# Kernel optimization log

Measured on AMD Instinct MI355X. Metric: run time of the kernel, lower is better.

Reference implementation:

```python
import jax, jax.numpy as jnp
import numpy as np

K = 20
EPS = 1e-5
SLOPE = 0.2


def knn_idx(x, k):
    # x: (B, C, N) -> (B, N, k) indices of k nearest neighbors (incl. self)
    xx = jnp.sum(x * x, axis=1)  # (B, N)
    # negative squared distance: largest = nearest
    pd = 2.0 * jnp.einsum('bcn,bcm->bnm', x, x) - xx[:, :, None] - xx[:, None, :]
    return jax.lax.top_k(pd, k)[1]


def graph_feature(x, k):
    # x: (B, C, N) -> (B, 2C, N, k) edge features [x_j - x_i, x_i]
    idx = knn_idx(x, k)                       # (B, N, k)
    xt = jnp.transpose(x, (0, 2, 1))          # (B, N, C)
    feat = jax.vmap(lambda xb, ib: xb[ib])(xt, idx)  # (B, N, k, C)
    center = xt[:, :, None, :]
    out = jnp.concatenate([feat - center, jnp.broadcast_to(center, feat.shape)], axis=-1)
    return jnp.transpose(out, (0, 3, 1, 2))   # (B, 2C, N, k)


def conv_bn_lrelu2d(x, W, g, b):
    # 1x1 Conv2d (no bias) + BatchNorm2d (batch stats, train mode) + LeakyReLU(0.2)
    y = jnp.einsum('oc,bcnk->bonk', W, x)
    m = jnp.mean(y, axis=(0, 2, 3), keepdims=True)
    v = jnp.var(y, axis=(0, 2, 3), keepdims=True)
    y = (y - m) * jax.lax.rsqrt(v + EPS) * g[None, :, None, None] + b[None, :, None, None]
    return jnp.where(y > 0, y, SLOPE * y)


def conv_bn_lrelu1d(x, W, g, b):
    y = jnp.einsum('oc,bcn->bon', W, x)
    m = jnp.mean(y, axis=(0, 2), keepdims=True)
    v = jnp.var(y, axis=(0, 2), keepdims=True)
    y = (y - m) * jax.lax.rsqrt(v + EPS) * g[None, :, None] + b[None, :, None]
    return jnp.where(y > 0, y, SLOPE * y)


def setup_inputs() -> dict:
    key = jax.random.key(0)
    ks = jax.random.split(key, 8)
    B, N, C = 8, 2048, 3
    emb = 1024
    fix = 1  # output == 'pointwise'
    xyz = jax.random.normal(ks[0], (B, N, C), dtype=jnp.float32)
    def w(k, o, i):
        return jax.random.normal(k, (o, i), dtype=jnp.float32) * (1.0 / np.sqrt(i))
    inp = {
        'xyz': xyz,
        'W1': w(ks[1], 64, 2 * C), 'g1': jnp.ones((64,), jnp.float32), 'b1': jnp.zeros((64,), jnp.float32),
        'W2': w(ks[2], 64, 128), 'g2': jnp.ones((64,), jnp.float32), 'b2': jnp.zeros((64,), jnp.float32),
        'W3': w(ks[3], 128, 128), 'g3': jnp.ones((128,), jnp.float32), 'b3': jnp.zeros((128,), jnp.float32),
        'W4': w(ks[4], 256 + fix, 256), 'g4': jnp.ones((256 + fix,), jnp.float32), 'b4': jnp.zeros((256 + fix,), jnp.float32),
        'W5': w(ks[5], emb, 512 + fix), 'g5': jnp.ones((emb,), jnp.float32), 'b5': jnp.zeros((emb,), jnp.float32),
    }
    return inp


def reference(xyz, W1, g1, b1, W2, g2, b2, W3, g3, b3, W4, g4, b4, W5, g5, b5):
    x0 = jnp.transpose(xyz, (0, 2, 1))  # (B, 3, N)
    B, _, N = x0.shape

    x = graph_feature(x0, K)            # (B, 6, N, k)
    x1 = jnp.max(conv_bn_lrelu2d(x, W1, g1, b1), axis=-1)   # (B, 64, N)

    x = graph_feature(x1, K)            # (B, 128, N, k)
    x2 = jnp.max(conv_bn_lrelu2d(x, W2, g2, b2), axis=-1)   # (B, 64, N)

    x = graph_feature(x2, K)            # (B, 128, N, k)
    x3 = jnp.max(conv_bn_lrelu2d(x, W3, g3, b3), axis=-1)   # (B, 128, N)

    x = graph_feature(x3, K)            # (B, 256, N, k)
    x4 = jnp.max(conv_bn_lrelu2d(x, W4, g4, b4), axis=-1)   # (B, 257, N)

    x_f = jnp.concatenate([x1, x2, x3, x4], axis=1)          # (B, 513, N)
    _x = conv_bn_lrelu1d(x_f, W5, g5, b5)                    # (B, emb, N)

    gmax = jnp.max(_x, axis=-1)   # (B, emb)
    gavg = jnp.mean(_x, axis=-1)  # (B, emb)
    g = jnp.concatenate([gmax, gavg], axis=1)[:, :, None]    # (B, 2*emb, 1)
    g = jnp.broadcast_to(g, (B, g.shape[1], N))
    return jnp.concatenate([g, x0, x_f], axis=1)             # (B, 2*emb+3+513, N)
```

## Files before the change

kernel.cpp:

```cpp
#include <hip/hip_runtime.h>
#include <math.h>

#define BB 8
#define NN 2048
#define KK 20
#define OCH 2564
#define OCN ((size_t)OCH*NN)
#define EPSD 1e-5
#define SLOPED 0.2
#define TS 64

#define WS_PD   ((size_t)0)
#define WS_YMX  ((size_t)4194304)
#define WS_YMN  ((size_t)8404992)
#define WS_U    ((size_t)12615680)
#define WS_V    ((size_t)16826368)
#define WS_IDX  ((size_t)21037056)
#define WS_XX   ((size_t)21364736)
#define WS_WTF  ((size_t)21381120)
#define WS_WTD  ((size_t)21426496)
#define WS_W5T  ((size_t)21471872)
#define WS_Y5   ((size_t)0)
#define WS_S1   ((size_t)21997184)
#define WS_S2   (WS_S1 + 2048)
#define WS_SC   (WS_S2 + 2048)
#define WS_SH   (WS_SC + 2048)

static inline int cdiv(int a, int b){ return (a+b-1)/b; }

__global__ void k_prep_x0(const float* __restrict__ xyz, float* __restrict__ out){
  int id = blockIdx.x*256 + threadIdx.x;
  if (id >= BB*NN) return;
  int b = id / NN, n = id % NN;
  const float* p = xyz + ((size_t)b*NN + n)*3;
  float* o = out + (size_t)b*OCN + (size_t)2048*NN + n;
  o[0] = p[0]; o[(size_t)NN] = p[1]; o[2*(size_t)NN] = p[2];
}

__global__ void k_wt_all(const float* __restrict__ W1, const float* __restrict__ W2,
                         const float* __restrict__ W3, const float* __restrict__ W4,
                         const float* __restrict__ W5,
                         float* __restrict__ wtf, float* __restrict__ wtd,
                         float* __restrict__ w5t){
  int id = blockIdx.x*256 + threadIdx.x;
  if (id < 513*1024){
    int c = id / 1024, o = id % 1024;
    w5t[(size_t)c*1024 + o] = W5[(size_t)o*513 + c];
  }
  if (id < 45376){
    const float* W; int C, O; int base;
    if (id < 192)        { W = W1; C = 3;   O = 64;  base = 0; }
    else if (id < 4288)  { W = W2; C = 64;  O = 64;  base = 192; }
    else if (id < 12480) { W = W3; C = 64;  O = 128; base = 4288; }
    else                 { W = W4; C = 128; O = 257; base = 12480; }
    int r = id - base;
    int c = r / O, o = r % O;
    float wf = W[(size_t)o*(2*C) + c];
    float wc = W[(size_t)o*(2*C) + C + c];
    wtf[base + (size_t)c*O + o] = wf;
    wtd[base + (size_t)c*O + o] = wc - wf;
  }
}

__global__ void k_xx32(const float* __restrict__ x, int C, size_t bs, float* __restrict__ xx,
                       double* __restrict__ s1, double* __restrict__ s2){
  if (blockIdx.x == 0 && blockIdx.y == 0){
    int t = threadIdx.x;
    #pragma unroll
    for (int i=0;i<4;i++){ s1[t*4+i] = 0.0; s2[t*4+i] = 0.0; }
  }
  int b = blockIdx.y;
  int n = blockIdx.x*256 + threadIdx.x;
  const float* p = x + (size_t)b*bs + n;
  float a;
  if (C <= 8){
    a = 0.f;
    for (int c = 0; c < C; c++){ float v = p[(size_t)c*NN]; float s = v*v; a = a + s; }
  } else {
    float r0,r1,r2,r3,r4,r5,r6,r7;
    { float v;
      v = p[0];            r0 = v*v;
      v = p[(size_t)1*NN]; r1 = v*v;
      v = p[(size_t)2*NN]; r2 = v*v;
      v = p[(size_t)3*NN]; r3 = v*v;
      v = p[(size_t)4*NN]; r4 = v*v;
      v = p[(size_t)5*NN]; r5 = v*v;
      v = p[(size_t)6*NN]; r6 = v*v;
      v = p[(size_t)7*NN]; r7 = v*v;
    }
    for (int i = 8; i < C; i += 8){
      float v;
      v = p[(size_t)(i+0)*NN]; r0 = r0 + v*v;
      v = p[(size_t)(i+1)*NN]; r1 = r1 + v*v;
      v = p[(size_t)(i+2)*NN]; r2 = r2 + v*v;
      v = p[(size_t)(i+3)*NN]; r3 = r3 + v*v;
      v = p[(size_t)(i+4)*NN]; r4 = r4 + v*v;
      v = p[(size_t)(i+5)*NN]; r5 = r5 + v*v;
      v = p[(size_t)(i+6)*NN]; r6 = r6 + v*v;
      v = p[(size_t)(i+7)*NN]; r7 = r7 + v*v;
    }
    a = ((r0+r1)+(r2+r3)) + ((r4+r5)+(r6+r7));
  }
  xx[b*NN + n] = a;
}

__global__ __launch_bounds__(256) void k_pd4(const float* __restrict__ x, int C, size_t bs, int b0,
                     const float* __restrict__ xx, float* __restrict__ wsbase,
                     unsigned long long o0, unsigned long long o1,
                     unsigned long long o2, unsigned long long o3){
  int z = blockIdx.z;
  unsigned long long off = (z==0)?o0:((z==1)?o1:((z==2)?o2:o3));
  float* pd = wsbase + off;
  int b = b0 + z;
  __shared__ float As[8][128];
  __shared__ float Bs[8][128];
  int n0 = blockIdx.y*128, m0 = blockIdx.x*128;
  int tid = threadIdx.x;
  int ty = tid / 16, tx = tid % 16;
  const float* xb = x + (size_t)b*bs;
  float acc[8][8] = {};
  for (int c0 = 0; c0 < C; c0 += 8){
    #pragma unroll
    for (int rr = 0; rr < 4; rr++){
      int t2 = tid + rr*256;
      int c = t2 >> 7, col = t2 & 127;
      int cc = c0 + c;
      float av = 0.f, bv = 0.f;
      if (cc < C){ av = xb[(size_t)cc*NN + n0 + col]; bv = xb[(size_t)cc*NN + m0 + col]; }
      As[c][col] = av; Bs[c][col] = bv;
    }
    __syncthreads();
    #pragma unroll
    for (int c = 0; c < 8; c++){
      float4 a0 = *reinterpret_cast<const float4*>(&As[c][ty*8]);
      float4 a1 = *reinterpret_cast<const float4*>(&As[c][ty*8+4]);
      float4 b0v = *reinterpret_cast<const float4*>(&Bs[c][tx*4]);
      float4 b1v = *reinterpret_cast<const float4*>(&Bs[c][64 + tx*4]);
      float a[8]  = {a0.x,a0.y,a0.z,a0.w,a1.x,a1.y,a1.z,a1.w};
      float bv[8] = {b0v.x,b0v.y,b0v.z,b0v.w,b1v.x,b1v.y,b1v.z,b1v.w};
      #pragma unroll
      for (int i=0;i<8;i++)
        #pragma unroll
        for (int j=0;j<8;j++)
          acc[i][j] = fmaf(a[i], bv[j], acc[i][j]);
    }
    __syncthreads();
  }
  const float* xxb = xx + b*NN;
  float xm0[4], xm1[4];
  #pragma unroll
  for (int j=0;j<4;j++){ xm0[j] = xxb[m0 + tx*4 + j]; xm1[j] = xxb[m0 + 64 + tx*4 + j]; }
  #pragma unroll
  for (int i=0;i<8;i++){
    int n = n0 + ty*8 + i;
    float xn = xxb[n];
    float4 v0, v1;
    v0.x = (2.f*acc[i][0] - xn) - xm0[0];
    v0.y = (2.f*acc[i][1] - xn) - xm0[1];
    v0.z = (2.f*acc[i][2] - xn) - xm0[2];
    v0.w = (2.f*acc[i][3] - xn) - xm0[3];
    v1.x = (2.f*acc[i][4] - xn) - xm1[0];
    v1.y = (2.f*acc[i][5] - xn) - xm1[1];
    v1.z = (2.f*acc[i][6] - xn) - xm1[2];
    v1.w = (2.f*acc[i][7] - xn) - xm1[3];
    *reinterpret_cast<float4*>(&pd[(size_t)n*NN + m0 + tx*4])      = v0;
    *reinterpret_cast<float4*>(&pd[(size_t)n*NN + m0 + 64 + tx*4]) = v1;
  }
}

__global__ __launch_bounds__(256) void k_topk4(const float* __restrict__ wsbase,
                     unsigned long long o0, unsigned long long o1,
                     unsigned long long o2, unsigned long long o3,
                     int b0, int* __restrict__ idx){
  int z = blockIdx.y;
  unsigned long long off = (z==0)?o0:((z==1)?o1:((z==2)?o2:o3));
  const float* pdb = wsbase + off;
  int b = b0 + z;
  int lane = threadIdx.x & 63;
  int w = threadIdx.x >> 6;
  int n = blockIdx.x*4 + w;
  const float* row = pdb + (size_t)n*NN;
  float vals[KK]; int inds[KK];
  #pragma unroll
  for (int i=0;i<KK;i++){ vals[i] = -INFINITY; inds[i] = NN; }
  for (int c = 0; c < NN/64; c++){
    int m = c*64 + lane;
    float v = row[m];
    if (v > vals[KK-1]){
      #pragma unroll
      for (int i=KK-1;i>0;--i){
        if (vals[i-1] < v){ vals[i]=vals[i-1]; inds[i]=inds[i-1]; }
      }
      bool done = false;
      #pragma unroll
      for (int i=0;i<KK;i++){
        bool pl = (!done) && (vals[i] < v);
        if (pl){ vals[i]=v; inds[i]=m; done=true; }
      }
    }
  }
  int* op = idx + ((size_t)b*NN + n)*KK;
  #pragma unroll 1
  for (int r = 0; r < KK; r++){
    float bv = vals[0]; int bi = inds[0];
    #pragma unroll
    for (int s = 1; s < 64; s <<= 1){
      float ov = __shfl_xor(bv, s);
      int   oi = __shfl_xor(bi, s);
      if (ov > bv || (ov == bv && oi < bi)){ bv = ov; bi = oi; }
    }
    if (inds[0] == bi){
      #pragma unroll
      for (int i=0;i<KK-1;i++){ vals[i]=vals[i+1]; inds[i]=inds[i+1]; }
      vals[KK-1] = -INFINITY; inds[KK-1] = NN;
    }
    if (lane == 0) op[r] = bi;
  }
}

__global__ __launch_bounds__(256) void k_gemm_uv(
    const float* __restrict__ x, int C, int O, size_t bs,
    const float* __restrict__ wtf, const float* __restrict__ wtd,
    float* __restrict__ u, float* __restrict__ v){
  __shared__ float Xs[8][TS];
  __shared__ float Wfs[8][TS];
  __shared__ float Wds[8][TS];
  int b = blockIdx.z;
  int n0 = blockIdx.y*TS, o0 = blockIdx.x*TS;
  int tid = threadIdx.x, tx = tid%16, ty = tid/16;
  const float* xb = x + (size_t)b*bs;
  double au[4][4] = {};
  double av[4][4] = {};
  for (int c0 = 0; c0 < C; c0 += 8){
    int r = tid/64, col = tid%64;
    #pragma unroll
    for (int rr=0;rr<2;rr++){
      int c = c0 + r + rr*4;
      float xv=0.f, wfv=0.f, wdv=0.f;
      if (c < C){
        xv = xb[(size_t)c*NN + n0 + col];
        if (o0+col < O){
          wfv = wtf[(size_t)c*O + o0+col];
          wdv = wtd[(size_t)c*O + o0+col];
        }
      }
      Xs[r+rr*4][col]=xv; Wfs[r+rr*4][col]=wfv; Wds[r+rr*4][col]=wdv;
    }
    __syncthreads();
    #pragma unroll
    for (int c=0;c<8;c++){
      double a[4], f[4], d[4];
      #pragma unroll
      for (int i=0;i<4;i++) a[i] = (double)Xs[c][ty*4+i];
      #pragma unroll
      for (int j=0;j<4;j++) f[j] = (double)Wfs[c][tx*4+j];
      #pragma unroll
      for (int j=0;j<4;j++) d[j] = (double)Wds[c][tx*4+j];
      #pragma unroll
      for (int i=0;i<4;i++)
        #pragma unroll
        for (int j=0;j<4;j++){
          au[i][j] = fma(a[i], f[j], au[i][j]);
          av[i][j] = fma(a[i], d[j], av[i][j]);
        }
    }
    __syncthreads();
  }
  #pragma unroll
  for (int i=0;i<4;i++){
    int n = n0 + ty*4 + i;
    #pragma unroll
    for (int j=0;j<4;j++){
      int o = o0 + tx*4 + j;
      if (o < O){
        u[((size_t)b*NN + n)*O + o] = (float)au[i][j];
        v[((size_t)b*NN + n)*O + o] = (float)av[i][j];
      }
    }
  }
}

#define NT 32
__global__ __launch_bounds__(256) void k_passB(
  const float* __restrict__ u, const float* __restrict__ v, const int* __restrict__ idx,
  int O, int OT, float* __restrict__ ymax, float* __restrict__ ymin,
  double* __restrict__ s1, double* __restrict__ s2){
  __shared__ int ids[NT*KK];
  int b = blockIdx.y, n0 = blockIdx.x*NT;
  int tid = threadIdx.x;
  for (int t = tid; t < NT*KK; t += 256) ids[t] = idx[((size_t)b*NN + n0)*KK + t];
  __syncthreads();
  int nsplit = 256/OT;
  int ob = tid % OT, ns = tid / OT;
  int nper = NT / nsplit;
  const float* ub = u + (size_t)b*NN*O;
  const float* vb = v + (size_t)b*NN*O;
  for (int o = ob; o < O; o += 256){
    double s1p = 0.0, s2p = 0.0;
    for (int ni = ns*nper; ni < (ns+1)*nper; ni++){
      double su=0.0, sq=0.0;
      float mx=-INFINITY, mn=INFINITY;
      #pragma unroll
      for (int k=0;k<KK;k++){
        int j = ids[ni*KK + k];
        float uu = ub[(size_t)j*O + o];
        double ud = (double)uu;
        su += ud; sq += ud*ud;
        mx = fmaxf(mx, uu); mn = fminf(mn, uu);
      }
      float vv = vb[(size_t)(n0+ni)*O + o];
      double vd = (double)vv;
      s1p += su + (double)KK*vd;
      s2p += sq + 2.0*vd*su + (double)KK*vd*vd;
      size_t yo = ((size_t)b*NN + n0 + ni)*O + o;
      ymax[yo] = mx + vv; ymin[yo] = mn + vv;
    }
    atomicAdd(&s1[o], s1p);
    atomicAdd(&s2[o], s2p);
  }
}

__global__ __launch_bounds__(256) void k_passD(const float* __restrict__ ymax,
  const float* __restrict__ ymin, const double* __restrict__ s1,
  const double* __restrict__ s2, const float* __restrict__ g,
  const float* __restrict__ bb, int O, double M, float* __restrict__ xout){
  __shared__ float t[64][65];
  __shared__ double s_sc[64], s_sh[64];
  int b = blockIdx.z, n0 = blockIdx.y*64, o0 = blockIdx.x*64;
  int tid = threadIdx.x;
  if (tid < 64){
    int o = o0 + tid;
    double sc = 0.0, sh = 0.0;
    if (o < O){
      double mean = s1[o]/M;
      double var  = s2[o]/M - mean*mean;
      sc = (double)g[o] / sqrt(var + EPSD);
      sh = (double)bb[o] - mean*sc;
    }
    s_sc[tid] = sc; s_sh[tid] = sh;
  }
  __syncthreads();
  int col = tid % 64, rr = tid / 64;
  int o = o0 + col;
  bool ov = (o < O);
  double sc = s_sc[col];
  double sh = s_sh[col];
  const float* src = (sc >= 0.0) ? ymax : ymin;
  for (int p = 0; p < 16; p++){
    int n = n0 + p*4 + rr;
    float y = ov ? src[((size_t)b*NN + n)*O + o] : 0.f;
    double z = sc*(double)y + sh;
    z = z > 0.0 ? z : SLOPED*z;
    t[p*4+rr][col] = (float)z;
  }
  __syncthreads();
  float* xb = xout + (size_t)b*OCN;
  for (int p = 0; p < 16; p++){
    int row = p*4 + rr;
    if (o0 + row < O) xb[(size_t)(o0+row)*NN + n0 + col] = t[col][row];
  }
}

__global__ __launch_bounds__(256) void k_conv5g(const float* __restrict__ xf,
                                                const float* __restrict__ w5t,
                                                float* __restrict__ y5){
  __shared__ float Wsh[8][128];
  __shared__ float Xs[8][128];
  int o0 = blockIdx.x*128, n0 = blockIdx.y*128, b = blockIdx.z;
  int tid = threadIdx.x;
  int ty = tid / 16, tx = tid % 16;
  const float* xb = xf + (size_t)b*OCN;
  float acc[8][8] = {};
  for (int c0 = 0; c0 < 513; c0 += 8){
    #pragma unroll
    for (int rr = 0; rr < 4; rr++){
      int t2 = tid + rr*256;
      int c = t2 >> 7, col = t2 & 127;
      int cc = c0 + c;
      float wv = 0.f, xv = 0.f;
      if (cc < 513){
        wv = w5t[(size_t)cc*1024 + o0 + col];
        xv = xb[(size_t)cc*NN + n0 + col];
      }
      Wsh[c][col] = wv; Xs[c][col] = xv;
    }
    __syncthreads();
    #pragma unroll
    for (int c = 0; c < 8; c++){
      float4 w0 = *reinterpret_cast<const float4*>(&Wsh[c][ty*8]);
      float4 w1 = *reinterpret_cast<const float4*>(&Wsh[c][ty*8+4]);
      float4 x0 = *reinterpret_cast<const float4*>(&Xs[c][tx*4]);
      float4 x1 = *reinterpret_cast<const float4*>(&Xs[c][64 + tx*4]);
      float wr[8] = {w0.x,w0.y,w0.z,w0.w,w1.x,w1.y,w1.z,w1.w};
      float xr[8] = {x0.x,x0.y,x0.z,x0.w,x1.x,x1.y,x1.z,x1.w};
      #pragma unroll
      for (int i=0;i<8;i++)
        #pragma unroll
        for (int j=0;j<8;j++)
          acc[i][j] = fmaf(wr[i], xr[j], acc[i][j]);
    }
    __syncthreads();
  }
  #pragma unroll
  for (int i=0;i<8;i++){
    int o = o0 + ty*8 + i;
    float* yr = y5 + ((size_t)b*1024 + o)*NN;
    float4 v0 = {acc[i][0], acc[i][1], acc[i][2], acc[i][3]};
    float4 v1 = {acc[i][4], acc[i][5], acc[i][6], acc[i][7]};
    *reinterpret_cast<float4*>(&yr[n0 + tx*4])      = v0;
    *reinterpret_cast<float4*>(&yr[n0 + 64 + tx*4]) = v1;
  }
}

__global__ __launch_bounds__(256) void k_stats5_v2(const float* __restrict__ y5,
                                                   const float* __restrict__ g,
                                                   const float* __restrict__ bb,
                                                   double* __restrict__ scale,
                                                   double* __restrict__ shift){
  int o = blockIdx.x;
  __shared__ double sh1[256], sh2[256];
  double a = 0.0, q = 0.0;
  for (int bn = threadIdx.x; bn < BB*NN; bn += 256){
    int b = bn >> 11, n = bn & 2047;
    double yv = (double)y5[((size_t)b*1024 + o)*NN + n];
    a += yv; q += yv*yv;
  }
  sh1[threadIdx.x] = a; sh2[threadIdx.x] = q;
  __syncthreads();
  for (int s = 128; s > 0; s >>= 1){
    if (threadIdx.x < s){ sh1[threadIdx.x] += sh1[threadIdx.x+s]; sh2[threadIdx.x] += sh2[threadIdx.x+s]; }
    __syncthreads();
  }
  if (threadIdx.x == 0){
    double M = (double)(BB*NN);
    double mean = sh1[0]/M;
    double var  = sh2[0]/M - mean*mean;
    double sc = (double)g[o]/sqrt(var + EPSD);
    scale[o] = sc;
    shift[o] = (double)bb[o] - mean*sc;
  }
}

__global__ __launch_bounds__(256) void k_final5_v2(const float* __restrict__ y5,
                                                   const double* __restrict__ scale,
                                                   const double* __restrict__ shift,
                                                   float* __restrict__ out){
  int o = blockIdx.x, b = blockIdx.y;
  __shared__ double smx[256], ssm[256];
  double sc = scale[o], sh = shift[o];
  double mx = -INFINITY, sm = 0.0;
  const float* yrow = y5 + ((size_t)b*1024 + o)*NN;
  for (int n = threadIdx.x; n < NN; n += 256){
    double z = sc*(double)yrow[n] + sh;
    z = z > 0.0 ? z : SLOPED*z;
    mx = fmax(mx, z); sm += z;
  }
  smx[threadIdx.x] = mx; ssm[threadIdx.x] = sm;
  __syncthreads();
  for (int s = 128; s > 0; s >>= 1){
    if (threadIdx.x < s){
      smx[threadIdx.x] = fmax(smx[threadIdx.x], smx[threadIdx.x+s]);
      ssm[threadIdx.x] += ssm[threadIdx.x+s];
    }
    __syncthreads();
  }
  float vg = (float)smx[0];
  float va = (float)(ssm[0]*(1.0/NN));
  float* ob = out + (size_t)b*OCN;
  for (int n = threadIdx.x; n < NN; n += 256){
    ob[(size_t)o*NN + n] = vg;
    ob[(size_t)(1024+o)*NN + n] = va;
  }
}

extern "C" void kernel_launch(void* const* d_in, const int* in_sizes, int n_in,
                              void* d_out, int out_size, void* d_ws, size_t ws_size,
                              hipStream_t stream){
  const float* xyz = (const float*)d_in[0];
  float* out = (float*)d_out;
  float* ws  = (float*)d_ws;

  const float* Wp[5] = {(const float*)d_in[1],(const float*)d_in[4],(const float*)d_in[7],(const float*)d_in[10],(const float*)d_in[13]};
  const float* Gp[5] = {(const float*)d_in[2],(const float*)d_in[5],(const float*)d_in[8],(const float*)d_in[11],(const float*)d_in[14]};
  const float* Bp[5] = {(const float*)d_in[3],(const float*)d_in[6],(const float*)d_in[9],(const float*)d_in[12],(const float*)d_in[15]};
  int Cin[4]  = {3, 64, 64, 128};
  int Oc[4]   = {64, 64, 128, 257};
  int xinc[4] = {2048, 2051, 2115, 2179};
  int xoutc[4]= {2051, 2115, 2179, 2307};
  int woff[4] = {0, 192, 4288, 12480};

  float* ymx  = ws + WS_YMX;
  float* ymn  = ws + WS_YMN;
  float* u    = ws + WS_U;
  float* v    = ws + WS_V;
  int*   idx  = (int*)(ws + WS_IDX);
  float* xx   = ws + WS_XX;
  float* wtf  = ws + WS_WTF;
  float* wtd  = ws + WS_WTD;
  float* w5t  = ws + WS_W5T;
  float* y5   = ws + WS_Y5;
  double* s1d = (double*)(ws + WS_S1);
  double* s2d = (double*)(ws + WS_S2);
  double* scd = (double*)(ws + WS_SC);
  double* shd = (double*)(ws + WS_SH);

  k_prep_x0<<<cdiv(BB*NN,256), 256, 0, stream>>>(xyz, out);
  k_wt_all <<<cdiv(513*1024,256), 256, 0, stream>>>(Wp[0], Wp[1], Wp[2], Wp[3], Wp[4], wtf, wtd, w5t);

  for (int t = 0; t < 4; t++){
    int C = Cin[t], O = Oc[t];
    const float* xin = out + (size_t)xinc[t]*NN;
    k_xx32<<<dim3(NN/256, BB), 256, 0, stream>>>(xin, C, OCN, xx, s1d, s2d);
    int OT = (O <= 64) ? 64 : ((O <= 128) ? 128 : 256);
    for (int bg = 0; bg < 2; bg++){
      k_pd4  <<<dim3(NN/128, NN/128, 4), 256, 0, stream>>>(xin, C, OCN, bg*4, xx, ws,
               (unsigned long long)WS_PD, (unsigned long long)WS_YMX,
               (unsigned long long)WS_YMN, (unsigned long long)WS_U);
      k_topk4<<<dim3(NN/4, 4), 256, 0, stream>>>(ws,
               (unsigned long long)WS_PD, (unsigned long long)WS_YMX,
               (unsigned long long)WS_YMN, (unsigned long long)WS_U,
               bg*4, idx);
    }
    k_gemm_uv<<<dim3(cdiv(O,TS), NN/TS, BB), 256, 0, stream>>>(xin, C, O, OCN, wtf + woff[t], wtd + woff[t], u, v);
    k_passB  <<<dim3(NN/NT, BB), 256, 0, stream>>>(u, v, idx, O, OT, ymx, ymn, s1d, s2d);
    k_passD  <<<dim3(cdiv(O,TS), NN/TS, BB), 256, 0, stream>>>(ymx, ymn, s1d, s2d, Gp[t], Bp[t], O,
               (double)((size_t)BB*NN*KK), out + (size_t)xoutc[t]*NN);
  }

  k_conv5g<<<dim3(1024/128, NN/128, BB), 256, 0, stream>>>(out + (size_t)2051*NN, w5t, y5);
  k_stats5_v2<<<1024, 256, 0, stream>>>(y5, Gp[4], Bp[4], scd, shd);
  k_final5_v2<<<dim3(1024, BB), 256, 0, stream>>>(y5, scd, shd, out);
}
```

Baseline: 2.422 ms.

## Fuse pairwise-distance GEMM with top-k selection into one kernel

Replaces the two-kernel path, which wrote full NxN distance matrices for groups of four batches and then scanned them for top-k, with a single kernel. Each block computes distances for 32 rows against all columns and keeps per-thread top-k lists in registers, merging them with an 8-lane shuffle reduction. This removes the large distance-matrix write and re-read and one launch per batch group. In exchange the GEMM tiling is less efficient (a 32-row tile with one A value per thread per step, Bs reloaded for every column chunk), the grid is only 512 blocks, and the insertion sort now sits inside the compute loop, which may cause divergence.

```diff
diff --git a/kernel.cpp b/kernel.cpp
--- a/kernel.cpp
+++ b/kernel.cpp
@@ -10,7 +10,6 @@
 #define SLOPED 0.2
 #define TS 64
 
-#define WS_PD   ((size_t)0)
 #define WS_YMX  ((size_t)4194304)
 #define WS_YMN  ((size_t)8404992)
 #define WS_U    ((size_t)12615680)
@@ -104,107 +103,89 @@
   xx[b*NN + n] = a;
 }
 
-__global__ __launch_bounds__(256) void k_pd4(const float* __restrict__ x, int C, size_t bs, int b0,
-                     const float* __restrict__ xx, float* __restrict__ wsbase,
-                     unsigned long long o0, unsigned long long o1,
-                     unsigned long long o2, unsigned long long o3){
-  int z = blockIdx.z;
-  unsigned long long off = (z==0)?o0:((z==1)?o1:((z==2)?o2:o3));
-  float* pd = wsbase + off;
-  int b = b0 + z;
-  __shared__ float As[8][128];
-  __shared__ float Bs[8][128];
-  int n0 = blockIdx.y*128, m0 = blockIdx.x*128;
+__global__ __launch_bounds__(256) void k_pdtopk(
+    const float* __restrict__ x, int C, size_t bs,
+    const float* __restrict__ xx, int* __restrict__ idx){
+  __shared__ float As[128][32];
+  __shared__ float Bs[8][256];
+  int b = blockIdx.y;
+  int r0 = blockIdx.x * 32;
   int tid = threadIdx.x;
-  int ty = tid / 16, tx = tid % 16;
+  int row = tid >> 3;
+  int mc  = tid & 7;
   const float* xb = x + (size_t)b*bs;
-  float acc[8][8] = {};
-  for (int c0 = 0; c0 < C; c0 += 8){
-    #pragma unroll
-    for (int rr = 0; rr < 4; rr++){
-      int t2 = tid + rr*256;
-      int c = t2 >> 7, col = t2 & 127;
-      int cc = c0 + c;
-      float av = 0.f, bv = 0.f;
-      if (cc < C){ av = xb[(size_t)cc*NN + n0 + col]; bv = xb[(size_t)cc*NN + m0 + col]; }
-      As[c][col] = av; Bs[c][col] = bv;
-    }
-    __syncthreads();
-    #pragma unroll
-    for (int c = 0; c < 8; c++){
-      float4 a0 = *reinterpret_cast<const float4*>(&As[c][ty*8]);
-      float4 a1 = *reinterpret_cast<const float4*>(&As[c][ty*8+4]);
-      float4 b0v = *reinterpret_cast<const float4*>(&Bs[c][tx*4]);
-      float4 b1v = *reinterpret_cast<const float4*>(&Bs[c][64 + tx*4]);
-      float a[8]  = {a0.x,a0.y,a0.z,a0.w,a1.x,a1.y,a1.z,a1.w};
-      float bv[8] = {b0v.x,b0v.y,b0v.z,b0v.w,b1v.x,b1v.y,b1v.z,b1v.w};
-      #pragma unroll
-      for (int i=0;i<8;i++)
-        #pragma unroll
-        for (int j=0;j<8;j++)
-          acc[i][j] = fmaf(a[i], bv[j], acc[i][j]);
-    }
-    __syncthreads();
-  }
   const float* xxb = xx + b*NN;
-  float xm0[4], xm1[4];
-  #pragma unroll
-  for (int j=0;j<4;j++){ xm0[j] = xxb[m0 + tx*4 + j]; xm1[j] = xxb[m0 + 64 + tx*4 + j]; }
-  #pragma unroll
-  for (int i=0;i<8;i++){
-    int n = n0 + ty*8 + i;
-    float xn = xxb[n];
-    float4 v0, v1;
-    v0.x = (2.f*acc[i][0] - xn) - xm0[0];
-    v0.y = (2.f*acc[i][1] - xn) - xm0[1];
-    v0.z = (2.f*acc[i][2] - xn) - xm0[2];
-    v0.w = (2.f*acc[i][3] - xn) - xm0[3];
-    v1.x = (2.f*acc[i][4] - xn) - xm1[0];
-    v1.y = (2.f*acc[i][5] - xn) - xm1[1];
-    v1.z = (2.f*acc[i][6] - xn) - xm1[2];
-    v1.w = (2.f*acc[i][7] - xn) - xm1[3];
-    *reinterpret_cast<float4*>(&pd[(size_t)n*NN + m0 + tx*4])      = v0;
-    *reinterpret_cast<float4*>(&pd[(size_t)n*NN + m0 + 64 + tx*4]) = v1;
-  }
-}
-
-__global__ __launch_bounds__(256) void k_topk4(const float* __restrict__ wsbase,
-                     unsigned long long o0, unsigned long long o1,
-                     unsigned long long o2, unsigned long long o3,
-                     int b0, int* __restrict__ idx){
-  int z = blockIdx.y;
-  unsigned long long off = (z==0)?o0:((z==1)?o1:((z==2)?o2:o3));
-  const float* pdb = wsbase + off;
-  int b = b0 + z;
-  int lane = threadIdx.x & 63;
-  int w = threadIdx.x >> 6;
-  int n = blockIdx.x*4 + w;
-  const float* row = pdb + (size_t)n*NN;
+  int Cpad = (C + 7) & ~7;
+  for (int t2 = tid; t2 < Cpad*32; t2 += 256){
+    int c = t2 >> 5, r = t2 & 31;
+    As[c][r] = (c < C) ? xb[(size_t)c*NN + r0 + r] : 0.f;
+  }
+  __syncthreads();
+  float xn = xxb[r0 + row];
   float vals[KK]; int inds[KK];
   #pragma unroll
   for (int i=0;i<KK;i++){ vals[i] = -INFINITY; inds[i] = NN; }
-  for (int c = 0; c < NN/64; c++){
-    int m = c*64 + lane;
-    float v = row[m];
-    if (v > vals[KK-1]){
-      #pragma unroll
-      for (int i=KK-1;i>0;--i){
-        if (vals[i-1] < v){ vals[i]=vals[i-1]; inds[i]=inds[i-1]; }
-      }
-      bool done = false;
-      #pragma unroll
-      for (int i=0;i<KK;i++){
-        bool pl = (!done) && (vals[i] < v);
-        if (pl){ vals[i]=v; inds[i]=m; done=true; }
-      }
-    }
-  }
-  int* op = idx + ((size_t)b*NN + n)*KK;
+  for (int mb = 0; mb < 8; mb++){
+    int mbase = mb*256;
+    float acc[8][4];
+    #pragma unroll
+    for (int q=0;q<8;q++){
+      #pragma unroll
+      for (int e=0;e<4;e++) acc[q][e] = 0.f;
+    }
+    for (int c0 = 0; c0 < C; c0 += 8){
+      #pragma unroll
+      for (int rr=0; rr<8; rr++){
+        int t2 = tid + rr*256;
+        int c = t2 >> 8, col = t2 & 255;
+        int cc = c0 + c;
+        Bs[c][col] = (cc < C) ? xb[(size_t)cc*NN + mbase + col] : 0.f;
+      }
+      __syncthreads();
+      #pragma unroll
+      for (int c=0;c<8;c++){
+        float a = As[c0+c][row];
+        #pragma unroll
+        for (int q=0;q<8;q++){
+          float4 bq = *reinterpret_cast<const float4*>(&Bs[c][q*32 + mc*4]);
+          acc[q][0] = fmaf(a, bq.x, acc[q][0]);
+          acc[q][1] = fmaf(a, bq.y, acc[q][1]);
+          acc[q][2] = fmaf(a, bq.z, acc[q][2]);
+          acc[q][3] = fmaf(a, bq.w, acc[q][3]);
+        }
+      }
+      __syncthreads();
+    }
+    #pragma unroll
+    for (int q=0;q<8;q++){
+      float4 xm = *reinterpret_cast<const float4*>(&xxb[mbase + q*32 + mc*4]);
+      float xmv[4] = {xm.x, xm.y, xm.z, xm.w};
+      #pragma unroll
+      for (int e=0;e<4;e++){
+        float t = 2.f*acc[q][e];
+        float v = (t - xn) - xmv[e];
+        if (v > vals[KK-1]){
+          int m = mbase + q*32 + mc*4 + e;
+          #pragma unroll
+          for (int i=KK-1;i>0;--i){
+            if (vals[i-1] < v){ vals[i]=vals[i-1]; inds[i]=inds[i-1]; }
+          }
+          bool done = false;
+          #pragma unroll
+          for (int i=0;i<KK;i++){
+            bool pl = (!done) && (vals[i] < v);
+            if (pl){ vals[i]=v; inds[i]=m; done=true; }
+          }
+        }
+      }
+    }
+  }
+  int* op = idx + ((size_t)b*NN + r0 + row)*KK;
   #pragma unroll 1
   for (int r = 0; r < KK; r++){
     float bv = vals[0]; int bi = inds[0];
     #pragma unroll
-    for (int s = 1; s < 64; s <<= 1){
+    for (int s = 1; s < 8; s <<= 1){
       float ov = __shfl_xor(bv, s);
       int   oi = __shfl_xor(bi, s);
       if (ov > bv || (ov == bv && oi < bi)){ bv = ov; bi = oi; }
@@ -214,7 +195,7 @@
       for (int i=0;i<KK-1;i++){ vals[i]=vals[i+1]; inds[i]=inds[i+1]; }
       vals[KK-1] = -INFINITY; inds[KK-1] = NN;
     }
-    if (lane == 0) op[r] = bi;
+    if (mc == 0) op[r] = bi;
   }
 }
 
@@ -512,15 +493,7 @@
     const float* xin = out + (size_t)xinc[t]*NN;
     k_xx32<<<dim3(NN/256, BB), 256, 0, stream>>>(xin, C, OCN, xx, s1d, s2d);
     int OT = (O <= 64) ? 64 : ((O <= 128) ? 128 : 256);
-    for (int bg = 0; bg < 2; bg++){
-      k_pd4  <<<dim3(NN/128, NN/128, 4), 256, 0, stream>>>(xin, C, OCN, bg*4, xx, ws,
-               (unsigned long long)WS_PD, (unsigned long long)WS_YMX,
-               (unsigned long long)WS_YMN, (unsigned long long)WS_U);
-      k_topk4<<<dim3(NN/4, 4), 256, 0, stream>>>(ws,
-               (unsigned long long)WS_PD, (unsigned long long)WS_YMX,
-               (unsigned long long)WS_YMN, (unsigned long long)WS_U,
-               bg*4, idx);
-    }
+    k_pdtopk<<<dim3(NN/32, BB), 256, 0, stream>>>(xin, C, OCN, xx, idx);
     k_gemm_uv<<<dim3(cdiv(O,TS), NN/TS, BB), 256, 0, stream>>>(xin, C, O, OCN, wtf + woff[t], wtd + woff[t], u, v);
     k_passB  <<<dim3(NN/NT, BB), 256, 0, stream>>>(u, v, idx, O, OT, ymx, ymn, s1d, s2d);
     k_passD  <<<dim3(cdiv(O,TS), NN/TS, BB), 256, 0, stream>>>(ymx, ymn, s1d, s2d, Gp[t], Bp[t], O,
```

After: 2.906 ms. 1.2x slower.
